# Kernel optimization log

Measured on AMD Instinct MI355X. Metric: run time of the kernel, lower is better.

## Reference

```python
import jax, jax.numpy as jnp
import numpy as np

B, N, K, D = 4, 32768, 16, 8  # batch, points, neighbors, output channels
EPS = 1e-6  # BatchNorm eps from module


def setup_inputs() -> dict:
    key = jax.random.key(0)
    ks = jax.random.split(key, 6)
    coords = jax.random.normal(ks[0], (B, N, 3), jnp.float32)
    features = jax.random.normal(ks[1], (B, D, N, 1), jnp.float32)
    knn_idx = jax.random.randint(ks[2], (B, N, K), 0, N, dtype=jnp.int64)
    knn_dist = jax.random.uniform(ks[3], (B, N, K), jnp.float32)
    mask = jnp.ones((B, N), jnp.int32)  # all-valid points
    conv_w = jax.random.normal(ks[4], (D, 10), jnp.float32) * 0.1  # 1x1 Conv2d weight (out,in)
    conv_b = jnp.zeros((D,), jnp.float32)
    bn_gamma = jnp.ones((D,), jnp.float32)
    bn_beta = jnp.zeros((D,), jnp.float32)
    return {
        "coords": coords, "features": features, "knn_idx": knn_idx,
        "knn_dist": knn_dist, "mask": mask, "conv_w": conv_w,
        "conv_b": conv_b, "bn_gamma": bn_gamma, "bn_beta": bn_beta,
    }


def reference(coords, features, knn_idx, knn_dist, mask, conv_w, conv_b, bn_gamma, bn_beta):
    # coords: (B,N,3); knn_idx/knn_dist: (B,N,K); features: (B,D,N,1); mask: (B,N)
    idx = jnp.clip(knn_idx, 0, None)
    # gather neighbor coords per batch: (B,N,K,3)
    neighbors = jax.vmap(lambda c, i: c[i])(coords, idx)
    center = jnp.broadcast_to(coords[:, :, None, :], neighbors.shape)  # (B,N,K,3)
    # masked_fill invalid points' distances with +inf (mask==0)
    dist = jnp.where(mask[:, :, None] == 0, jnp.inf, knn_dist)
    # channel-last concat: [center(3), neighbors(3), diff(3), dist(1)] -> (B,N,K,10)
    feat = jnp.concatenate(
        [center, neighbors, center - neighbors, dist[..., None]], axis=-1)
    # 1x1 conv == per-position linear 10 -> D, output layout (B,D,N,K)
    x = jnp.einsum('bnkc,dc->bdnk', feat, conv_w) + conv_b[None, :, None, None]
    # BatchNorm2d in training mode: biased batch stats over (B,N,K) per channel
    mean = x.mean(axis=(0, 2, 3), keepdims=True)
    var = x.var(axis=(0, 2, 3), keepdims=True)
    x = (x - mean) * jax.lax.rsqrt(var + EPS)
    x = x * bn_gamma[None, :, None, None] + bn_beta[None, :, None, None]
    x = jax.nn.relu(x)
    # expand features (B,D,N,1) -> (B,D,N,K) and concat on channel dim
    f = jnp.broadcast_to(features, (x.shape[0], features.shape[1], x.shape[2], x.shape[3]))
    return jnp.concatenate([x, f], axis=1)  # (B, 2D, N, K)
```

## Files before the change

kernel.cpp:

```cpp
#include <hip/hip_runtime.h>

#define NB 4
#define NP 32768
#define NK 16
#define ND 8
#define EPSV 1e-6f


__global__ __launch_bounds__(256) void lse_stats(
    const float* __restrict__ coords,
    const int*   __restrict__ knn_idx,
    const float* __restrict__ knn_dist,
    const int*   __restrict__ mask,
    const float* __restrict__ conv_w,
    const float* __restrict__ conv_b,
    float*       __restrict__ accum)
{
    const int gid = blockIdx.x * 256 + threadIdx.x;
    const int b   = gid >> 17;
    const int r   = gid & (NP * 4 - 1);
    const int n   = r >> 2;
    const int k0  = (r & 3) * 4;

    float a0[ND], a1[ND], a2[ND], e0[ND], e1[ND], e2[ND], w9[ND], cb[ND];
#pragma unroll
    for (int d = 0; d < ND; ++d) {
        const float* w = conv_w + d * 10;
        a0[d] = w[0] + w[6]; a1[d] = w[1] + w[7]; a2[d] = w[2] + w[8];
        e0[d] = w[3] - w[6]; e1[d] = w[4] - w[7]; e2[d] = w[5] - w[8];
        w9[d] = w[9];        cb[d] = conv_b[d];
    }

    const float* cbase = coords + (size_t)b * NP * 3;
    const float  cx = cbase[n * 3 + 0];
    const float  cy = cbase[n * 3 + 1];
    const float  cz = cbase[n * 3 + 2];

    const size_t p  = ((size_t)(b * NP + n)) * NK + k0;
    const int4   id = *(const int4*)(knn_idx + p);
    float4       dv = *(const float4*)(knn_dist + p);
    if (mask[b * NP + n] == 0) {
        dv.x = dv.y = dv.z = dv.w = __builtin_inff();
    }

    const int   js[4] = {id.x < 0 ? 0 : id.x, id.y < 0 ? 0 : id.y,
                         id.z < 0 ? 0 : id.z, id.w < 0 ? 0 : id.w};
    const float ds[4] = {dv.x, dv.y, dv.z, dv.w};

    float sum[ND], sq[ND];
#pragma unroll
    for (int d = 0; d < ND; ++d) { sum[d] = 0.f; sq[d] = 0.f; }

#pragma unroll
    for (int t = 0; t < 4; ++t) {
        const float* nb = cbase + (size_t)js[t] * 3;
        const float  nx = nb[0], ny = nb[1], nz = nb[2];
#pragma unroll
        for (int d = 0; d < ND; ++d) {
            float x = fmaf(a0[d], cx, fmaf(a1[d], cy, fmaf(a2[d], cz,
                      fmaf(e0[d], nx, fmaf(e1[d], ny, fmaf(e2[d], nz,
                      fmaf(w9[d], ds[t], cb[d])))))));
            sum[d] += x;
            sq[d]   = fmaf(x, x, sq[d]);
        }
    }

#pragma unroll
    for (int d = 0; d < ND; ++d) {
        float s = sum[d], s2 = sq[d];
#pragma unroll
        for (int off = 32; off > 0; off >>= 1) {
            s  += __shfl_down(s,  off);
            s2 += __shfl_down(s2, off);
        }
        sum[d] = s; sq[d] = s2;
    }
    __shared__ float lds[4][16];
    const int wave = threadIdx.x >> 6, lane = threadIdx.x & 63;
    if (lane == 0) {
#pragma unroll
        for (int d = 0; d < ND; ++d) {
            lds[wave][d]     = sum[d];
            lds[wave][8 + d] = sq[d];
        }
    }
    __syncthreads();
    if (threadIdx.x < 16) {
        float v = lds[0][threadIdx.x] + lds[1][threadIdx.x]
                + lds[2][threadIdx.x] + lds[3][threadIdx.x];
        atomicAdd(&accum[threadIdx.x], v);
    }
}

__global__ __launch_bounds__(256) void lse_write(
    const float* __restrict__ coords,
    const float* __restrict__ features,
    const int*   __restrict__ knn_idx,
    const float* __restrict__ knn_dist,
    const int*   __restrict__ mask,
    const float* __restrict__ conv_w,
    const float* __restrict__ conv_b,
    const float* __restrict__ accum,
    const float* __restrict__ bn_gamma,
    const float* __restrict__ bn_beta,
    float*       __restrict__ out)
{
    const int gid = blockIdx.x * 256 + threadIdx.x;
    const int b   = gid >> 17;
    const int r   = gid & (NP * 4 - 1);
    const int n   = r >> 2;
    const int k0  = (r & 3) * 4;

    const float invM = 1.0f / (float)(NB * NP * NK);
    float a0[ND], a1[ND], a2[ND], e0[ND], e1[ND], e2[ND], w9[ND], cb[ND];
#pragma unroll
    for (int d = 0; d < ND; ++d) {
        const float* w = conv_w + d * 10;
        const float mean = accum[d] * invM;
        const float var  = fmaf(-mean, mean, accum[8 + d] * invM);
        const float g    = bn_gamma[d] * rsqrtf(var + EPSV);
        const float sh   = fmaf(-mean, g, bn_beta[d]);
        a0[d] = (w[0] + w[6]) * g; a1[d] = (w[1] + w[7]) * g; a2[d] = (w[2] + w[8]) * g;
        e0[d] = (w[3] - w[6]) * g; e1[d] = (w[4] - w[7]) * g; e2[d] = (w[5] - w[8]) * g;
        w9[d] = w[9] * g;          cb[d] = fmaf(conv_b[d], g, sh);
    }

    const float* cbase = coords + (size_t)b * NP * 3;
    const float  cx = cbase[n * 3 + 0];
    const float  cy = cbase[n * 3 + 1];
    const float  cz = cbase[n * 3 + 2];

    const size_t p  = ((size_t)(b * NP + n)) * NK + k0;
    const int4   id = *(const int4*)(knn_idx + p);
    float4       dv = *(const float4*)(knn_dist + p);
    if (mask[b * NP + n] == 0) {
        dv.x = dv.y = dv.z = dv.w = __builtin_inff();
    }

    const int   js[4] = {id.x < 0 ? 0 : id.x, id.y < 0 ? 0 : id.y,
                         id.z < 0 ? 0 : id.z, id.w < 0 ? 0 : id.w};
    const float ds[4] = {dv.x, dv.y, dv.z, dv.w};

    float xv[4][ND];
#pragma unroll
    for (int t = 0; t < 4; ++t) {
        const float* nb = cbase + (size_t)js[t] * 3;
        const float  nx = nb[0], ny = nb[1], nz = nb[2];
#pragma unroll
        for (int d = 0; d < ND; ++d) {
            xv[t][d] = fmaf(a0[d], cx, fmaf(a1[d], cy, fmaf(a2[d], cz,
                       fmaf(e0[d], nx, fmaf(e1[d], ny, fmaf(e2[d], nz,
                       fmaf(w9[d], ds[t], cb[d])))))));
        }
    }

#pragma unroll
    for (int d = 0; d < ND; ++d) {
        float4 v;
        v.x = fmaxf(xv[0][d], 0.f);
        v.y = fmaxf(xv[1][d], 0.f);
        v.z = fmaxf(xv[2][d], 0.f);
        v.w = fmaxf(xv[3][d], 0.f);
        *(float4*)(out + ((((size_t)(b * 2 * ND + d)) * NP + n) << 4) + k0) = v;
    }

    const float* fb = features + (size_t)b * ND * NP;
#pragma unroll
    for (int d = 0; d < ND; ++d) {
        const float v = fb[d * NP + n];
        *(float4*)(out + ((((size_t)(b * 2 * ND + ND + d)) * NP + n) << 4) + k0) =
            make_float4(v, v, v, v);
    }
}

extern "C" void kernel_launch(void* const* d_in, const int* in_sizes, int n_in,
                              void* d_out, int out_size, void* d_ws, size_t ws_size,
                              hipStream_t stream) {
    const float* coords   = (const float*)d_in[0];
    const float* features = (const float*)d_in[1];
    const int*   knn_idx  = (const int*)  d_in[2];
    const float* knn_dist = (const float*)d_in[3];
    const int*   mask     = (const int*)  d_in[4];
    const float* conv_w   = (const float*)d_in[5];
    const float* conv_b   = (const float*)d_in[6];
    const float* bn_gamma = (const float*)d_in[7];
    const float* bn_beta  = (const float*)d_in[8];
    float* out   = (float*)d_out;
    float* accum = (float*)d_ws;

    hipMemsetAsync(d_ws, 0, 64, stream);

    lse_stats<<<(NB * NP * 4) / 256, 256, 0, stream>>>(
        coords, knn_idx, knn_dist, mask, conv_w, conv_b, accum);

    lse_write<<<(NB * NP * 4) / 256, 256, 0, stream>>>(
        coords, features, knn_idx, knn_dist, mask, conv_w, conv_b,
        accum, bn_gamma, bn_beta, out);
}
```

Baseline: 213.4 us.

## Fuse BN stats and write passes into one cooperative kernel with grid sync

Replaces the two-pass stats/write launch with a single cooperative kernel that computes the conv outputs once, keeps them in registers as packed fp16, accumulates batch statistics, grid-syncs, then normalizes and writes. This removes the second read of indices, distances and gathered neighbor coordinates. Atomics are spread over four accumulator slots to reduce contention, and the feature broadcast writes are issued before the sync. It risks fp16 rounding error in the stored pre-norm values and depends on the cooperative launch fitting all 2048 blocks, falling back to the old two-kernel path otherwise.

```diff
diff --git a/kernel.cpp b/kernel.cpp
--- a/kernel.cpp
+++ b/kernel.cpp
@@ -1,4 +1,6 @@
 #include <hip/hip_runtime.h>
+#include <hip/hip_cooperative_groups.h>
+#include <hip/hip_fp16.h>
 
 #define NB 4
 #define NP 32768
@@ -6,6 +8,153 @@
 #define ND 8
 #define EPSV 1e-6f
 
+namespace cg = cooperative_groups;
+
+
+__global__ __launch_bounds__(256, 8) void lse_fused(
+    const float* __restrict__ coords,
+    const float* __restrict__ features,
+    const int*   __restrict__ knn_idx,
+    const float* __restrict__ knn_dist,
+    const int*   __restrict__ mask,
+    const float* __restrict__ conv_w,
+    const float* __restrict__ conv_b,
+    const float* __restrict__ bn_gamma,
+    const float* __restrict__ bn_beta,
+    float*       __restrict__ accum,
+    float*       __restrict__ out)
+{
+    const int gid = blockIdx.x * 256 + threadIdx.x;
+    const int b   = gid >> 17;
+    const int r   = gid & (NP * 4 - 1);
+    const int n   = r >> 2;
+    const int k0  = (r & 3) * 4;
+
+    const float* cbase = coords + (size_t)b * NP * 3;
+    const float  cx = cbase[n * 3 + 0];
+    const float  cy = cbase[n * 3 + 1];
+    const float  cz = cbase[n * 3 + 2];
+
+    const size_t p  = ((size_t)(b * NP + n)) * NK + k0;
+    const int4   id = *(const int4*)(knn_idx + p);
+    float4       dv = *(const float4*)(knn_dist + p);
+    if (mask[b * NP + n] == 0) {
+        dv.x = dv.y = dv.z = dv.w = __builtin_inff();
+    }
+    const int   js[4] = {id.x < 0 ? 0 : id.x, id.y < 0 ? 0 : id.y,
+                         id.z < 0 ? 0 : id.z, id.w < 0 ? 0 : id.w};
+    const float ds4[4] = {dv.x, dv.y, dv.z, dv.w};
+
+    float nbx[4], nby[4], nbz[4];
+#pragma unroll
+    for (int t = 0; t < 4; ++t) {
+        const float* nb = cbase + (size_t)js[t] * 3;
+        nbx[t] = nb[0]; nby[t] = nb[1]; nbz[t] = nb[2];
+    }
+
+    float sum[ND], sq[ND];
+#pragma unroll
+    for (int d = 0; d < ND; ++d) { sum[d] = 0.f; sq[d] = 0.f; }
+
+    uint32_t xp[4][4];
+#pragma unroll
+    for (int dp = 0; dp < 4; ++dp) {
+        const int d0 = 2 * dp, d1 = d0 + 1;
+        const float* wA = conv_w + d0 * 10;
+        const float* wB = conv_w + d1 * 10;
+        const float aA0 = wA[0] + wA[6], aA1 = wA[1] + wA[7], aA2 = wA[2] + wA[8];
+        const float eA0 = wA[3] - wA[6], eA1 = wA[4] - wA[7], eA2 = wA[5] - wA[8];
+        const float wA9 = wA[9],         cbA = conv_b[d0];
+        const float aB0 = wB[0] + wB[6], aB1 = wB[1] + wB[7], aB2 = wB[2] + wB[8];
+        const float eB0 = wB[3] - wB[6], eB1 = wB[4] - wB[7], eB2 = wB[5] - wB[8];
+        const float wB9 = wB[9],         cbB = conv_b[d1];
+#pragma unroll
+        for (int t = 0; t < 4; ++t) {
+            float xA = fmaf(aA0, cx, fmaf(aA1, cy, fmaf(aA2, cz,
+                       fmaf(eA0, nbx[t], fmaf(eA1, nby[t], fmaf(eA2, nbz[t],
+                       fmaf(wA9, ds4[t], cbA)))))));
+            float xB = fmaf(aB0, cx, fmaf(aB1, cy, fmaf(aB2, cz,
+                       fmaf(eB0, nbx[t], fmaf(eB1, nby[t], fmaf(eB2, nbz[t],
+                       fmaf(wB9, ds4[t], cbB)))))));
+            sum[d0] += xA; sq[d0] = fmaf(xA, xA, sq[d0]);
+            sum[d1] += xB; sq[d1] = fmaf(xB, xB, sq[d1]);
+            __half2 h = __floats2half2_rn(xA, xB);
+            xp[t][dp] = *(const uint32_t*)&h;
+        }
+    }
+
+    const float* fb = features + (size_t)b * ND * NP;
+#pragma unroll
+    for (int d = 0; d < ND; ++d) {
+        const float v = fb[d * NP + n];
+        *(float4*)(out + ((((size_t)(b * 2 * ND + ND + d)) * NP + n) << 4) + k0) =
+            make_float4(v, v, v, v);
+    }
+
+#pragma unroll
+    for (int d = 0; d < ND; ++d) {
+        float s = sum[d], s2 = sq[d];
+#pragma unroll
+        for (int off = 32; off > 0; off >>= 1) {
+            s  += __shfl_down(s,  off);
+            s2 += __shfl_down(s2, off);
+        }
+        sum[d] = s; sq[d] = s2;
+    }
+    __shared__ float lred[4][16];
+    const int wave = threadIdx.x >> 6, lane = threadIdx.x & 63;
+    if (lane == 0) {
+#pragma unroll
+        for (int d = 0; d < ND; ++d) {
+            lred[wave][d]     = sum[d];
+            lred[wave][8 + d] = sq[d];
+        }
+    }
+    __syncthreads();
+    if (threadIdx.x < 16) {
+        float v = lred[0][threadIdx.x] + lred[1][threadIdx.x]
+                + lred[2][threadIdx.x] + lred[3][threadIdx.x];
+        atomicAdd(&accum[(blockIdx.x & 3) * 16 + threadIdx.x], v);
+    }
+
+    cg::this_grid().sync();
+
+    float av = __hip_atomic_load(&accum[lane], __ATOMIC_RELAXED,
+                                 __HIP_MEMORY_SCOPE_AGENT);
+    float fs[ND], fq[ND];
+#pragma unroll
+    for (int i = 0; i < ND; ++i) {
+        fs[i] = __shfl(av, i)     + __shfl(av, 16 + i)
+              + __shfl(av, 32 + i) + __shfl(av, 48 + i);
+        fq[i] = __shfl(av, 8 + i)  + __shfl(av, 24 + i)
+              + __shfl(av, 40 + i) + __shfl(av, 56 + i);
+    }
+
+    const float invM = 1.0f / (float)(NB * NP * NK);
+#pragma unroll
+    for (int dp = 0; dp < 4; ++dp) {
+        const int d0 = 2 * dp, d1 = d0 + 1;
+        const float m0 = fs[d0] * invM;
+        const float v0 = fmaf(-m0, m0, fq[d0] * invM);
+        const float g0 = bn_gamma[d0] * rsqrtf(v0 + EPSV);
+        const float s0 = fmaf(-m0, g0, bn_beta[d0]);
+        const float m1 = fs[d1] * invM;
+        const float v1 = fmaf(-m1, m1, fq[d1] * invM);
+        const float g1 = bn_gamma[d1] * rsqrtf(v1 + EPSV);
+        const float s1 = fmaf(-m1, g1, bn_beta[d1]);
+
+        float4 y0, y1;
+#pragma unroll
+        for (int t = 0; t < 4; ++t) {
+            __half2 h; *(uint32_t*)&h = xp[t][dp];
+            float2 f = __half22float2(h);
+            (&y0.x)[t] = fmaxf(fmaf(f.x, g0, s0), 0.f);
+            (&y1.x)[t] = fmaxf(fmaf(f.y, g1, s1), 0.f);
+        }
+        *(float4*)(out + ((((size_t)(b * 2 * ND + d0)) * NP + n) << 4) + k0) = y0;
+        *(float4*)(out + ((((size_t)(b * 2 * ND + d1)) * NP + n) << 4) + k0) = y1;
+    }
+}
 
 __global__ __launch_bounds__(256) void lse_stats(
     const float* __restrict__ coords,
@@ -32,63 +181,50 @@
     }
 
     const float* cbase = coords + (size_t)b * NP * 3;
-    const float  cx = cbase[n * 3 + 0];
-    const float  cy = cbase[n * 3 + 1];
-    const float  cz = cbase[n * 3 + 2];
-
+    const float cx = cbase[n*3], cy = cbase[n*3+1], cz = cbase[n*3+2];
     const size_t p  = ((size_t)(b * NP + n)) * NK + k0;
     const int4   id = *(const int4*)(knn_idx + p);
     float4       dv = *(const float4*)(knn_dist + p);
-    if (mask[b * NP + n] == 0) {
-        dv.x = dv.y = dv.z = dv.w = __builtin_inff();
-    }
-
+    if (mask[b * NP + n] == 0) dv.x = dv.y = dv.z = dv.w = __builtin_inff();
     const int   js[4] = {id.x < 0 ? 0 : id.x, id.y < 0 ? 0 : id.y,
                          id.z < 0 ? 0 : id.z, id.w < 0 ? 0 : id.w};
-    const float ds[4] = {dv.x, dv.y, dv.z, dv.w};
+    const float ds4[4] = {dv.x, dv.y, dv.z, dv.w};
 
     float sum[ND], sq[ND];
 #pragma unroll
     for (int d = 0; d < ND; ++d) { sum[d] = 0.f; sq[d] = 0.f; }
-
 #pragma unroll
     for (int t = 0; t < 4; ++t) {
         const float* nb = cbase + (size_t)js[t] * 3;
-        const float  nx = nb[0], ny = nb[1], nz = nb[2];
+        const float nx = nb[0], ny = nb[1], nz = nb[2];
 #pragma unroll
         for (int d = 0; d < ND; ++d) {
             float x = fmaf(a0[d], cx, fmaf(a1[d], cy, fmaf(a2[d], cz,
                       fmaf(e0[d], nx, fmaf(e1[d], ny, fmaf(e2[d], nz,
-                      fmaf(w9[d], ds[t], cb[d])))))));
-            sum[d] += x;
-            sq[d]   = fmaf(x, x, sq[d]);
-        }
-    }
-
+                      fmaf(w9[d], ds4[t], cb[d])))))));
+            sum[d] += x; sq[d] = fmaf(x, x, sq[d]);
+        }
+    }
 #pragma unroll
     for (int d = 0; d < ND; ++d) {
         float s = sum[d], s2 = sq[d];
 #pragma unroll
         for (int off = 32; off > 0; off >>= 1) {
-            s  += __shfl_down(s,  off);
-            s2 += __shfl_down(s2, off);
+            s += __shfl_down(s, off); s2 += __shfl_down(s2, off);
         }
         sum[d] = s; sq[d] = s2;
     }
-    __shared__ float lds[4][16];
+    __shared__ float lred[4][16];
     const int wave = threadIdx.x >> 6, lane = threadIdx.x & 63;
     if (lane == 0) {
 #pragma unroll
-        for (int d = 0; d < ND; ++d) {
-            lds[wave][d]     = sum[d];
-            lds[wave][8 + d] = sq[d];
-        }
+        for (int d = 0; d < ND; ++d) { lred[wave][d] = sum[d]; lred[wave][8+d] = sq[d]; }
     }
     __syncthreads();
     if (threadIdx.x < 16) {
-        float v = lds[0][threadIdx.x] + lds[1][threadIdx.x]
-                + lds[2][threadIdx.x] + lds[3][threadIdx.x];
-        atomicAdd(&accum[threadIdx.x], v);
+        float v = lred[0][threadIdx.x] + lred[1][threadIdx.x]
+                + lred[2][threadIdx.x] + lred[3][threadIdx.x];
+        atomicAdd(&accum[(blockIdx.x & 3) * 16 + threadIdx.x], v);
     }
 }
 
@@ -110,60 +246,55 @@
     const int r   = gid & (NP * 4 - 1);
     const int n   = r >> 2;
     const int k0  = (r & 3) * 4;
-
+    const int lane = threadIdx.x & 63;
+
+    float av = accum[lane];
+    float fs[ND], fq[ND];
+#pragma unroll
+    for (int i = 0; i < ND; ++i) {
+        fs[i] = __shfl(av, i) + __shfl(av, 16+i) + __shfl(av, 32+i) + __shfl(av, 48+i);
+        fq[i] = __shfl(av, 8+i) + __shfl(av, 24+i) + __shfl(av, 40+i) + __shfl(av, 56+i);
+    }
     const float invM = 1.0f / (float)(NB * NP * NK);
     float a0[ND], a1[ND], a2[ND], e0[ND], e1[ND], e2[ND], w9[ND], cb[ND];
 #pragma unroll
     for (int d = 0; d < ND; ++d) {
         const float* w = conv_w + d * 10;
-        const float mean = accum[d] * invM;
-        const float var  = fmaf(-mean, mean, accum[8 + d] * invM);
+        const float mean = fs[d] * invM;
+        const float var  = fmaf(-mean, mean, fq[d] * invM);
         const float g    = bn_gamma[d] * rsqrtf(var + EPSV);
         const float sh   = fmaf(-mean, g, bn_beta[d]);
-        a0[d] = (w[0] + w[6]) * g; a1[d] = (w[1] + w[7]) * g; a2[d] = (w[2] + w[8]) * g;
-        e0[d] = (w[3] - w[6]) * g; e1[d] = (w[4] - w[7]) * g; e2[d] = (w[5] - w[8]) * g;
-        w9[d] = w[9] * g;          cb[d] = fmaf(conv_b[d], g, sh);
+        a0[d] = (w[0]+w[6])*g; a1[d] = (w[1]+w[7])*g; a2[d] = (w[2]+w[8])*g;
+        e0[d] = (w[3]-w[6])*g; e1[d] = (w[4]-w[7])*g; e2[d] = (w[5]-w[8])*g;
+        w9[d] = w[9]*g;        cb[d] = fmaf(conv_b[d], g, sh);
     }
 
     const float* cbase = coords + (size_t)b * NP * 3;
-    const float  cx = cbase[n * 3 + 0];
-    const float  cy = cbase[n * 3 + 1];
-    const float  cz = cbase[n * 3 + 2];
-
+    const float cx = cbase[n*3], cy = cbase[n*3+1], cz = cbase[n*3+2];
     const size_t p  = ((size_t)(b * NP + n)) * NK + k0;
     const int4   id = *(const int4*)(knn_idx + p);
     float4       dv = *(const float4*)(knn_dist + p);
-    if (mask[b * NP + n] == 0) {
-        dv.x = dv.y = dv.z = dv.w = __builtin_inff();
-    }
-
+    if (mask[b * NP + n] == 0) dv.x = dv.y = dv.z = dv.w = __builtin_inff();
     const int   js[4] = {id.x < 0 ? 0 : id.x, id.y < 0 ? 0 : id.y,
                          id.z < 0 ? 0 : id.z, id.w < 0 ? 0 : id.w};
-    const float ds[4] = {dv.x, dv.y, dv.z, dv.w};
-
-    float xv[4][ND];
+    const float ds4[4] = {dv.x, dv.y, dv.z, dv.w};
+
 #pragma unroll
     for (int t = 0; t < 4; ++t) {
         const float* nb = cbase + (size_t)js[t] * 3;
-        const float  nx = nb[0], ny = nb[1], nz = nb[2];
+        const float nx = nb[0], ny = nb[1], nz = nb[2];
+        float xv[ND];
 #pragma unroll
         for (int d = 0; d < ND; ++d) {
-            xv[t][d] = fmaf(a0[d], cx, fmaf(a1[d], cy, fmaf(a2[d], cz,
-                       fmaf(e0[d], nx, fmaf(e1[d], ny, fmaf(e2[d], nz,
-                       fmaf(w9[d], ds[t], cb[d])))))));
-        }
-    }
-
-#pragma unroll
-    for (int d = 0; d < ND; ++d) {
-        float4 v;
-        v.x = fmaxf(xv[0][d], 0.f);
-        v.y = fmaxf(xv[1][d], 0.f);
-        v.z = fmaxf(xv[2][d], 0.f);
-        v.w = fmaxf(xv[3][d], 0.f);
-        *(float4*)(out + ((((size_t)(b * 2 * ND + d)) * NP + n) << 4) + k0) = v;
-    }
-
+            xv[d] = fmaxf(fmaf(a0[d], cx, fmaf(a1[d], cy, fmaf(a2[d], cz,
+                    fmaf(e0[d], nx, fmaf(e1[d], ny, fmaf(e2[d], nz,
+                    fmaf(w9[d], ds4[t], cb[d]))))))), 0.f);
+        }
+#pragma unroll
+        for (int d = 0; d < ND; ++d) {
+            out[((((size_t)(b * 2 * ND + d)) * NP + n) << 4) + k0 + t] = xv[d];
+        }
+    }
     const float* fb = features + (size_t)b * ND * NP;
 #pragma unroll
     for (int d = 0; d < ND; ++d) {
@@ -188,12 +319,22 @@
     float* out   = (float*)d_out;
     float* accum = (float*)d_ws;
 
-    hipMemsetAsync(d_ws, 0, 64, stream);
-
-    lse_stats<<<(NB * NP * 4) / 256, 256, 0, stream>>>(
-        coords, knn_idx, knn_dist, mask, conv_w, conv_b, accum);
-
-    lse_write<<<(NB * NP * 4) / 256, 256, 0, stream>>>(
-        coords, features, knn_idx, knn_dist, mask, conv_w, conv_b,
-        accum, bn_gamma, bn_beta, out);
+    hipMemsetAsync(d_ws, 0, 256, stream);
+
+    void* args[] = {
+        (void*)&coords, (void*)&features, (void*)&knn_idx, (void*)&knn_dist,
+        (void*)&mask, (void*)&conv_w, (void*)&conv_b, (void*)&bn_gamma,
+        (void*)&bn_beta, (void*)&accum, (void*)&out,
+    };
+    hipError_t e = hipLaunchCooperativeKernel(
+        (const void*)lse_fused, dim3(2048), dim3(256), args, 0, stream);
+
+    if (e != hipSuccess) {
+        (void)hipGetLastError();
+        lse_stats<<<2048, 256, 0, stream>>>(
+            coords, knn_idx, knn_dist, mask, conv_w, conv_b, accum);
+        lse_write<<<2048, 256, 0, stream>>>(
+            coords, features, knn_idx, knn_dist, mask, conv_w, conv_b,
+            accum, bn_gamma, bn_beta, out);
+    }
 }
```

Result: slower. 515.4 us (+141.5%).
